# Kernel optimization log

Measured on AMD Instinct MI355X. Metric: run time of the kernel, lower is better.

The kernel has to match this reference:

```python
import jax, jax.numpy as jnp
import numpy as np

N_CLASSES = 64
TRANSDUCTIVE_STEPS = 5


def setup_inputs() -> dict:
    key = jax.random.key(0)
    k1, k2, k3, k4 = jax.random.split(key, 4)
    support = jax.random.normal(k1, (1280, 2048), dtype=jnp.float32)
    query = jax.random.normal(k2, (65536, 2048), dtype=jnp.float32)
    support_labels = jax.random.randint(k3, (1280,), 0, N_CLASSES)
    W_enc = jax.random.normal(k4, (2048, 1024), dtype=jnp.float32) * 0.02
    b_enc = jnp.zeros((1024,), dtype=jnp.float32)
    return {"support": support, "query": query, "support_labels": support_labels,
            "W_enc": W_enc, "b_enc": b_enc}


def _segment_mean(emb, labels, n_seg):
    # masked-mean per class; empty classes stay zero (sum=0 / 1)
    sums = jax.ops.segment_sum(emb, labels, num_segments=n_seg)
    counts = jax.ops.segment_sum(jnp.ones((emb.shape[0],), emb.dtype), labels,
                                 num_segments=n_seg)
    return sums / jnp.maximum(counts, 1.0)[:, None]


def _cdist(x, p):
    # euclidean distance [n, d] x [c, d] -> [n, c]
    d2 = (jnp.sum(x * x, -1)[:, None] + jnp.sum(p * p, -1)[None, :]
          - 2.0 * x @ p.T)
    return jnp.sqrt(jnp.maximum(d2, 1e-12))


def reference(support, query, support_labels, W_enc, b_enc):
    support_emb = support @ W_enc + b_enc   # [ns, d]
    query_emb = query @ W_enc + b_enc       # [nq, d]

    prototypes = _segment_mean(support_emb, support_labels, N_CLASSES)
    all_emb = jnp.concatenate([support_emb, query_emb], axis=0)
    for _ in range(TRANSDUCTIVE_STEPS):
        query_labels = jnp.argmin(_cdist(query_emb, prototypes), axis=-1)
        all_labels = jnp.concatenate([support_labels, query_labels], axis=0)
        prototypes = _segment_mean(all_emb, all_labels, N_CLASSES)

    logits = -_cdist(query_emb, prototypes)  # [nq, n_classes]
    return logits
```

## Files before the change

### kernel.cpp

```cpp
#include <hip/hip_runtime.h>
#include <hip/hip_bf16.h>

#define NS 1280
#define NQ 65536
#define NA (NS + NQ)
#define DIN 2048
#define DEMB 1024
#define NC 64
#define STEPS 5
#define NDBLK (NQ / 128)

typedef __attribute__((ext_vector_type(8))) __bf16 bf16x8;
typedef __attribute__((ext_vector_type(4))) float f32x4;
typedef unsigned short u16;

__device__ __forceinline__ float b2f(u16 u) {
  return __uint_as_float(((unsigned int)u) << 16);
}
__device__ __forceinline__ u16 f2b(float f) {
  __hip_bfloat16 h = __float2bfloat16(f);
  u16 u; __builtin_memcpy(&u, &h, 2); return u;
}
__device__ __forceinline__ void gld_lds16(const void* g, void* l) {
  __builtin_amdgcn_global_load_lds(
      (const __attribute__((address_space(1))) void*)g,
      (__attribute__((address_space(3))) void*)l, 16, 0, 0);
}

__global__ __launch_bounds__(256) void cvt_bf16(const float4* __restrict__ in,
                                                ushort4* __restrict__ out, int n4) {
  for (int i = blockIdx.x * 256 + threadIdx.x; i < n4; i += gridDim.x * 256) {
    float4 v = in[i];
    ushort4 o;
    o.x = f2b(v.x); o.y = f2b(v.y); o.z = f2b(v.z); o.w = f2b(v.w);
    out[i] = o;
  }
}

__global__ __launch_bounds__(256) void transpose_w(const float* __restrict__ W,
                                                   u16* __restrict__ Wt) {
  __shared__ float tile[32][33];
  const int bx = blockIdx.x;
  const int by = blockIdx.y;
  const int tx = threadIdx.x & 31, ty = threadIdx.x >> 5;
#pragma unroll
  for (int j = 0; j < 4; j++)
    tile[ty + 8 * j][tx] = W[(size_t)(by * 32 + ty + 8 * j) * DEMB + bx * 32 + tx];
  __syncthreads();
#pragma unroll
  for (int j = 0; j < 4; j++)
    Wt[(size_t)(bx * 32 + ty + 8 * j) * DIN + by * 32 + tx] = f2b(tile[tx][ty + 8 * j]);
}

__global__ __launch_bounds__(256) void encoder_gemm(const u16* __restrict__ A,
                                                    const u16* __restrict__ Bt,
                                                    const float* __restrict__ bias,
                                                    u16* __restrict__ C) {
  const int b = blockIdx.x;
  const int x = b & 7, tt = b >> 3;
  const int mblk = x + 8 * (tt >> 3);
  const int nblk = tt & 7;
  if (mblk >= NA / 128) return;

  __shared__ u16 As[128 * 32];
  __shared__ u16 Bs[128 * 32];
  const int m0 = mblk * 128, n0 = nblk * 128;
  const int t = threadIdx.x;
  const int w = t >> 6, l = t & 63;
  const int lr = l & 15, lk = (l >> 4) * 8;
  const int wm = (w >> 1) * 64, wn = (w & 1) * 64;

  f32x4 acc[4][4];
  f32x4 z; z.x = 0.f; z.y = 0.f; z.z = 0.f; z.w = 0.f;
#pragma unroll
  for (int i = 0; i < 4; i++)
#pragma unroll
    for (int j = 0; j < 4; j++) acc[i][j] = z;

  const int rA0 = t >> 2, k8 = (t & 3) * 8;
  const u16* gA = A + (size_t)(m0 + rA0) * DIN + k8;
  const u16* gB = Bt + (size_t)(n0 + rA0) * DIN + k8;
  u16* lA = As + t * 8;
  u16* lB = Bs + t * 8;

  for (int kb = 0; kb < DIN; kb += 32) {
    gld_lds16(gA + kb, lA);
    gld_lds16(gA + kb + (size_t)64 * DIN, lA + 64 * 32);
    gld_lds16(gB + kb, lB);
    gld_lds16(gB + kb + (size_t)64 * DIN, lB + 64 * 32);
    __syncthreads();
    bf16x8 af[4], bf[4];
#pragma unroll
    for (int mt = 0; mt < 4; mt++) af[mt] = *(const bf16x8*)&As[(wm + mt * 16 + lr) * 32 + lk];
#pragma unroll
    for (int nt = 0; nt < 4; nt++) bf[nt] = *(const bf16x8*)&Bs[(wn + nt * 16 + lr) * 32 + lk];
#pragma unroll
    for (int mt = 0; mt < 4; mt++)
#pragma unroll
      for (int nt = 0; nt < 4; nt++)
        acc[mt][nt] = __builtin_amdgcn_mfma_f32_16x16x32_bf16(af[mt], bf[nt], acc[mt][nt], 0, 0, 0);
    __syncthreads();
  }
#pragma unroll
  for (int mt = 0; mt < 4; mt++)
#pragma unroll
    for (int nt = 0; nt < 4; nt++)
#pragma unroll
      for (int r = 0; r < 4; r++) {
        int row = m0 + wm + mt * 16 + (l >> 4) * 4 + r;
        int col = n0 + wn + nt * 16 + lr;
        float v = acc[mt][nt][r] + bias[col];
        C[(size_t)row * DEMB + col] = f2b(v);
      }
}

__global__ __launch_bounds__(256) void support_sums(const u16* __restrict__ emb,
                                                    const int* __restrict__ slab,
                                                    float* __restrict__ ssum,
                                                    int* __restrict__ scount) {
  const int c = blockIdx.x, t = threadIdx.x;
  __shared__ int lab[NS];
  for (int i = t; i < NS; i += 256) lab[i] = slab[i];
  __syncthreads();
  float a0 = 0, a1 = 0, a2 = 0, a3 = 0;
  int cnt = 0;
  for (int i = 0; i < NS; i++) {
    if (lab[i] == c) {
      ushort4 e = *(const ushort4*)&emb[(size_t)i * DEMB + t * 4];
      a0 += b2f(e.x); a1 += b2f(e.y); a2 += b2f(e.z); a3 += b2f(e.w);
      cnt++;
    }
  }
  float* dst = ssum + (size_t)c * DEMB + t * 4;
  dst[0] = a0; dst[1] = a1; dst[2] = a2; dst[3] = a3;
  if (t == 0) scount[c] = cnt;
}

__global__ __launch_bounds__(256) void qnorm_kernel(const u16* __restrict__ Q,
                                                    float* __restrict__ qnorm) {
  const int t = threadIdx.x, w = t >> 6, l = t & 63;
  const int row = blockIdx.x * 4 + w;
  const u16* p = Q + (size_t)row * DEMB;
  float s = 0.f;
#pragma unroll
  for (int kk = 0; kk < 4; kk++) {
    ushort4 e = *(const ushort4*)&p[kk * 256 + l * 4];
    float x0 = b2f(e.x), x1 = b2f(e.y), x2 = b2f(e.z), x3 = b2f(e.w);
    s += x0 * x0 + x1 * x1 + x2 * x2 + x3 * x3;
  }
#pragma unroll
  for (int d = 32; d >= 1; d >>= 1) s += __shfl_xor(s, d);
  if (l == 0) qnorm[row] = s;
}

template <bool INIT>
__global__ __launch_bounds__(256) void finalize_protos(const float* __restrict__ ssum,
                                                       const int* __restrict__ scount,
                                                       const float* __restrict__ qpart,
                                                       const int* __restrict__ histpart,
                                                       u16* __restrict__ protos,
                                                       float* __restrict__ pnorm) {
  const int c = blockIdx.x, t = threadIdx.x;
  __shared__ int wredi[4];
  __shared__ float wredf[4];
  __shared__ int cnt_sh;
  float inv;
  if (INIT) {
    inv = 1.0f / fmaxf((float)scount[c], 1.0f);
  } else {
    int p = histpart[(size_t)c * NDBLK + t] + histpart[(size_t)c * NDBLK + 256 + t];
#pragma unroll
    for (int d = 32; d >= 1; d >>= 1) p += __shfl_xor(p, d);
    if ((t & 63) == 0) wredi[t >> 6] = p;
    __syncthreads();
    if (t == 0) cnt_sh = scount[c] + wredi[0] + wredi[1] + wredi[2] + wredi[3];
    __syncthreads();
    inv = 1.0f / fmaxf((float)cnt_sh, 1.0f);
  }
  float part = 0.f;
#pragma unroll
  for (int j = 0; j < 4; j++) {
    const int d = t * 4 + j;
    float v = ssum[(size_t)c * DEMB + d];
    if (!INIT) {
#pragma unroll
      for (int ch = 0; ch < 8; ch++)
        v += qpart[((size_t)ch * NC + c) * DEMB + d];
    }
    v *= inv;
    u16 bits = f2b(v);
    protos[(size_t)c * DEMB + d] = bits;
    float vb = b2f(bits);
    part += vb * vb;
  }
#pragma unroll
  for (int d = 32; d >= 1; d >>= 1) part += __shfl_xor(part, d);
  if ((t & 63) == 0) wredf[t >> 6] = part;
  __syncthreads();
  if (t == 0) pnorm[c] = wredf[0] + wredf[1] + wredf[2] + wredf[3];
}

template <int MODE>
__global__ __launch_bounds__(256) void dist_kernel(const u16* __restrict__ Q,
                                                   const u16* __restrict__ P,
                                                   const float* __restrict__ pnorm,
                                                   const float* __restrict__ qnorm,
                                                   int* __restrict__ labels,
                                                   int* __restrict__ histpart,
                                                   float* __restrict__ out) {
  __shared__ u16 As[128 * 32];
  __shared__ u16 Bs[64 * 32];
  __shared__ int hist[NC];
  const int t = threadIdx.x;
  if (MODE == 0 && t < NC) hist[t] = 0;
  const int m0 = blockIdx.x * 128;
  const int w = t >> 6, l = t & 63;
  const int lr = l & 15, lk = (l >> 4) * 8;
  const int wm = w * 32;

  f32x4 acc[2][4];
  f32x4 z; z.x = 0.f; z.y = 0.f; z.z = 0.f; z.w = 0.f;
#pragma unroll
  for (int i = 0; i < 2; i++)
#pragma unroll
    for (int j = 0; j < 4; j++) acc[i][j] = z;

  const int rA0 = t >> 2, k8 = (t & 3) * 8;
  const u16* gA = Q + (size_t)(m0 + rA0) * DEMB + k8;
  const u16* gB = P + (size_t)rA0 * DEMB + k8;
  u16* lA = As + t * 8;
  u16* lB = Bs + t * 8;

  for (int kb = 0; kb < DEMB; kb += 32) {
    gld_lds16(gA + kb, lA);
    gld_lds16(gA + kb + (size_t)64 * DEMB, lA + 64 * 32);
    gld_lds16(gB + kb, lB);
    __syncthreads();
    bf16x8 af[2], bf[4];
#pragma unroll
    for (int mt = 0; mt < 2; mt++) af[mt] = *(const bf16x8*)&As[(wm + mt * 16 + lr) * 32 + lk];
#pragma unroll
    for (int nt = 0; nt < 4; nt++) bf[nt] = *(const bf16x8*)&Bs[(nt * 16 + lr) * 32 + lk];
#pragma unroll
    for (int mt = 0; mt < 2; mt++)
#pragma unroll
      for (int nt = 0; nt < 4; nt++)
        acc[mt][nt] = __builtin_amdgcn_mfma_f32_16x16x32_bf16(af[mt], bf[nt], acc[mt][nt], 0, 0, 0);
    __syncthreads();
  }

  if (MODE == 0) {
#pragma unroll
    for (int mt = 0; mt < 2; mt++)
#pragma unroll
      for (int r = 0; r < 4; r++) {
        float best = 3.402e38f; int bc = 0;
#pragma unroll
        for (int nt = 0; nt < 4; nt++) {
          int col = nt * 16 + lr;
          float v = pnorm[col] - 2.0f * acc[mt][nt][r];
          if (v < best) { best = v; bc = col; }
        }
#pragma unroll
        for (int s = 1; s < 16; s <<= 1) {
          float ov = __shfl_xor(best, s);
          int oc = __shfl_xor(bc, s);
          if (ov < best || (ov == best && oc < bc)) { best = ov; bc = oc; }
        }
        if (lr == 0) {
          int row = m0 + wm + mt * 16 + (l >> 4) * 4 + r;
          labels[row] = bc;
          atomicAdd(&hist[bc], 1);
        }
      }
    __syncthreads();
    if (t < NC) histpart[(size_t)t * NDBLK + blockIdx.x] = hist[t];
  } else {
#pragma unroll
    for (int mt = 0; mt < 2; mt++)
#pragma unroll
      for (int nt = 0; nt < 4; nt++)
#pragma unroll
        for (int r = 0; r < 4; r++) {
          int row = m0 + wm + mt * 16 + (l >> 4) * 4 + r;
          int col = nt * 16 + lr;
          float d2 = qnorm[row] + pnorm[col] - 2.0f * acc[mt][nt][r];
          out[(size_t)row * NC + col] = -sqrtf(fmaxf(d2, 1e-12f));
        }
  }
}

__global__ __launch_bounds__(256) void class_gather_sum(const u16* __restrict__ Q,
                                                        const int* __restrict__ labels,
                                                        float* __restrict__ qpart) {
  const int c = blockIdx.x >> 3;
  const int chunk = blockIdx.x & 7;
  const int base = chunk * (NQ / 8);
  const int t = threadIdx.x;
  __shared__ int list[NQ / 8];
  __shared__ int nmatch;
  if (t == 0) nmatch = 0;
  __syncthreads();
  for (int i = t; i < NQ / 8; i += 256) {
    if (labels[base + i] == c) {
      int p = atomicAdd(&nmatch, 1);
      list[p] = base + i;
    }
  }
  __syncthreads();
  const int cnt = nmatch;
  float a0 = 0, a1 = 0, a2 = 0, a3 = 0;
  for (int j = 0; j < cnt; j++) {
    int row = list[j];
    ushort4 e = *(const ushort4*)&Q[(size_t)row * DEMB + t * 4];
    a0 += b2f(e.x); a1 += b2f(e.y); a2 += b2f(e.z); a3 += b2f(e.w);
  }
  float* dst = qpart + ((size_t)chunk * NC + c) * DEMB + t * 4;
  dst[0] = a0; dst[1] = a1; dst[2] = a2; dst[3] = a3;
}

extern "C" void kernel_launch(void* const* d_in, const int* in_sizes, int n_in,
                              void* d_out, int out_size, void* d_ws, size_t ws_size,
                              hipStream_t stream) {
  const float* support = (const float*)d_in[0];
  const float* query   = (const float*)d_in[1];
  const int*   slab    = (const int*)d_in[2];
  const float* W       = (const float*)d_in[3];
  const float* bias    = (const float*)d_in[4];
  float* out = (float*)d_out;

  u16* Abf = (u16*)d_ws;
  u16* Wt  = Abf + (size_t)NA * DIN;
  u16* emb = Wt + (size_t)DEMB * DIN;
  float* ssum  = (float*)(emb + (size_t)NA * DEMB);
  float* pnorm = ssum + (size_t)NC * DEMB;
  float* qnorm = pnorm + NC;
  int* scount  = (int*)(qnorm + NQ);
  int* labels  = scount + NC;
  u16* protos  = (u16*)(labels + NQ);
  float* qpart = (float*)Abf;
  int* histpart = (int*)(qpart + (size_t)8 * NC * DEMB);

  const u16* Qemb = emb + (size_t)NS * DEMB;

  cvt_bf16<<<2048, 256, 0, stream>>>((const float4*)support, (ushort4*)Abf,
                                     NS * DIN / 4);
  cvt_bf16<<<8192, 256, 0, stream>>>((const float4*)query,
                                     (ushort4*)(Abf + (size_t)NS * DIN),
                                     NQ * DIN / 4);
  transpose_w<<<dim3(32, 64), 256, 0, stream>>>(W, Wt);

  encoder_gemm<<<8 * 66 * 8, 256, 0, stream>>>(Abf, Wt, bias, emb);

  support_sums<<<NC, 256, 0, stream>>>(emb, slab, ssum, scount);
  qnorm_kernel<<<NQ / 4, 256, 0, stream>>>(Qemb, qnorm);

  finalize_protos<true><<<NC, 256, 0, stream>>>(ssum, scount, qpart, histpart,
                                                protos, pnorm);

  for (int it = 0; it < STEPS; ++it) {
    dist_kernel<0><<<NDBLK, 256, 0, stream>>>(Qemb, protos, pnorm, nullptr,
                                              labels, histpart, nullptr);
    class_gather_sum<<<NC * 8, 256, 0, stream>>>(Qemb, labels, qpart);
    finalize_protos<false><<<NC, 256, 0, stream>>>(ssum, scount, qpart, histpart,
                                                   protos, pnorm);
  }

  dist_kernel<1><<<NDBLK, 256, 0, stream>>>(Qemb, protos, pnorm, qnorm,
                                            nullptr, nullptr, out);
}
```

Before: 1.532 ms.

## Rewrite encoder GEMM with 256x256 tiles, double-buffered swizzled LDS and interleaved prefetch

The encoder GEMM moves from 128x128 tiles with 256 threads and a K-step of 32 to 256x256 tiles with 512 threads and a K-step of 64. Shared memory is double-buffered with XOR-swizzled layout, and the next tile's global-to-LDS loads are interleaved between MFMA phases using explicit waitcnt, barriers and setprio. The aim is more reuse per loaded byte, fewer LDS bank conflicts, and hiding load latency behind compute. In exchange it uses 128KB of LDS and more registers per block, which lowers occupancy, and the hand-placed barrier scheduling is fragile.

```diff
diff --git a/kernel.cpp b/kernel.cpp
--- a/kernel.cpp
+++ b/kernel.cpp
@@ -52,66 +52,142 @@
     Wt[(size_t)(bx * 32 + ty + 8 * j) * DIN + by * 32 + tx] = f2b(tile[tx][ty + 8 * j]);
 }
 
-__global__ __launch_bounds__(256) void encoder_gemm(const u16* __restrict__ A,
-                                                    const u16* __restrict__ Bt,
-                                                    const float* __restrict__ bias,
-                                                    u16* __restrict__ C) {
+__device__ __forceinline__ void mm16(const bf16x8 af[4], const bf16x8 bf[4],
+                                     f32x4 (&acc)[4][4]) {
+#pragma unroll
+  for (int mt = 0; mt < 4; ++mt)
+#pragma unroll
+    for (int nt = 0; nt < 4; ++nt)
+      acc[mt][nt] = __builtin_amdgcn_mfma_f32_16x16x32_bf16(af[mt], bf[nt],
+                                                            acc[mt][nt], 0, 0, 0);
+}
+
+__global__ __launch_bounds__(512, 2) void encoder_gemm(const u16* __restrict__ A,
+                                                       const u16* __restrict__ Bt,
+                                                       const float* __restrict__ bias,
+                                                       u16* __restrict__ C) {
   const int b = blockIdx.x;
   const int x = b & 7, tt = b >> 3;
-  const int mblk = x + 8 * (tt >> 3);
-  const int nblk = tt & 7;
-  if (mblk >= NA / 128) return;
-
-  __shared__ u16 As[128 * 32];
-  __shared__ u16 Bs[128 * 32];
-  const int m0 = mblk * 128, n0 = nblk * 128;
+  const int mblk = x + 8 * (tt >> 2);
+  const int nblk = tt & 3;
+  if (mblk >= NA / 256) return;
+
+  __shared__ u16 lds[65536];
+
+  const int m0 = mblk * 256, n0 = nblk * 256;
   const int t = threadIdx.x;
   const int w = t >> 6, l = t & 63;
-  const int lr = l & 15, lk = (l >> 4) * 8;
-  const int wm = (w >> 1) * 64, wn = (w & 1) * 64;
-
-  f32x4 acc[4][4];
+  const int wm = (w >> 2) * 128;
+  const int wn = (w & 3) * 64;
+  const int lr = l & 15, lk8 = (l >> 4) * 8;
+  const int swz = (lr & 7) << 3;
+
+  const int c1 = t + 512;
+  const int r0 = t >> 3, r1 = c1 >> 3;
+  const int sc0 = (((t & 7) ^ (r0 & 7)) << 3);
+  const int sc1 = (((c1 & 7) ^ (r1 & 7)) << 3);
+
+  const u16* gAt = A + (size_t)m0 * DIN;
+  const u16* gBt = Bt + (size_t)n0 * DIN;
+
+  f32x4 acc[2][4][4];
   f32x4 z; z.x = 0.f; z.y = 0.f; z.z = 0.f; z.w = 0.f;
 #pragma unroll
-  for (int i = 0; i < 4; i++)
-#pragma unroll
-    for (int j = 0; j < 4; j++) acc[i][j] = z;
-
-  const int rA0 = t >> 2, k8 = (t & 3) * 8;
-  const u16* gA = A + (size_t)(m0 + rA0) * DIN + k8;
-  const u16* gB = Bt + (size_t)(n0 + rA0) * DIN + k8;
-  u16* lA = As + t * 8;
-  u16* lB = Bs + t * 8;
-
-  for (int kb = 0; kb < DIN; kb += 32) {
-    gld_lds16(gA + kb, lA);
-    gld_lds16(gA + kb + (size_t)64 * DIN, lA + 64 * 32);
-    gld_lds16(gB + kb, lB);
-    gld_lds16(gB + kb + (size_t)64 * DIN, lB + 64 * 32);
-    __syncthreads();
-    bf16x8 af[4], bf[4];
-#pragma unroll
-    for (int mt = 0; mt < 4; mt++) af[mt] = *(const bf16x8*)&As[(wm + mt * 16 + lr) * 32 + lk];
-#pragma unroll
-    for (int nt = 0; nt < 4; nt++) bf[nt] = *(const bf16x8*)&Bs[(wn + nt * 16 + lr) * 32 + lk];
-#pragma unroll
-    for (int mt = 0; mt < 4; mt++)
-#pragma unroll
-      for (int nt = 0; nt < 4; nt++)
-        acc[mt][nt] = __builtin_amdgcn_mfma_f32_16x16x32_bf16(af[mt], bf[nt], acc[mt][nt], 0, 0, 0);
-    __syncthreads();
-  }
-#pragma unroll
-  for (int mt = 0; mt < 4; mt++)
-#pragma unroll
-    for (int nt = 0; nt < 4; nt++)
-#pragma unroll
-      for (int r = 0; r < 4; r++) {
-        int row = m0 + wm + mt * 16 + (l >> 4) * 4 + r;
-        int col = n0 + wn + nt * 16 + lr;
-        float v = acc[mt][nt][r] + bias[col];
-        C[(size_t)row * DEMB + col] = f2b(v);
-      }
+  for (int g = 0; g < 2; ++g)
+#pragma unroll
+    for (int i = 0; i < 4; ++i)
+#pragma unroll
+      for (int j = 0; j < 4; ++j) acc[g][i][j] = z;
+
+  auto STAGE = [&](const u16* g, u16* S, int h, int kb) {
+    gld_lds16(g + (size_t)(h * 128 + r0) * DIN + kb + sc0, S + h * 8192 + t * 8);
+    gld_lds16(g + (size_t)(h * 128 + r1) * DIN + kb + sc1, S + h * 8192 + c1 * 8);
+  };
+
+  STAGE(gAt, lds, 0, 0);
+  STAGE(gAt, lds, 1, 0);
+  STAGE(gBt, lds + 16384, 0, 0);
+  STAGE(gBt, lds + 16384, 1, 0);
+
+  const int NT = DIN / 64;
+  for (int tk = 0; tk < NT; ++tk) {
+    const int p = tk & 1;
+    u16* LA = lds + p * 32768;
+    u16* LB = LA + 16384;
+    u16* SA = lds + (p ^ 1) * 32768;
+    u16* SB = SA + 16384;
+    const int kbn = (tk + 1) * 64;
+    const bool pre = (tk + 1 < NT);
+
+    bf16x8 af[4], bf0[4], bf1[4];
+
+    if (pre) {
+      STAGE(gAt, SA, 0, kbn);
+      asm volatile("s_waitcnt vmcnt(2)" ::: "memory");
+    } else {
+      asm volatile("s_waitcnt vmcnt(0)" ::: "memory");
+    }
+    __builtin_amdgcn_s_barrier();
+#pragma unroll
+    for (int mt = 0; mt < 4; ++mt)
+      af[mt] = *(const bf16x8*)&LA[(wm + mt * 16 + lr) * 64 + (lk8 ^ swz)];
+#pragma unroll
+    for (int nt = 0; nt < 4; ++nt)
+      bf0[nt] = *(const bf16x8*)&LB[(wn + nt * 16 + lr) * 64 + (lk8 ^ swz)];
+    __builtin_amdgcn_s_setprio(1);
+    mm16(af, bf0, acc[0]);
+    __builtin_amdgcn_s_setprio(0);
+    __builtin_amdgcn_s_barrier();
+
+#pragma unroll
+    for (int mt = 0; mt < 4; ++mt)
+      af[mt] = *(const bf16x8*)&LA[(wm + 64 + mt * 16 + lr) * 64 + (lk8 ^ swz)];
+    if (pre) STAGE(gAt, SA, 1, kbn);
+    __builtin_amdgcn_s_barrier();
+    __builtin_amdgcn_s_setprio(1);
+    mm16(af, bf0, acc[1]);
+    __builtin_amdgcn_s_setprio(0);
+    __builtin_amdgcn_s_barrier();
+
+#pragma unroll
+    for (int mt = 0; mt < 4; ++mt)
+      af[mt] = *(const bf16x8*)&LA[(wm + mt * 16 + lr) * 64 + ((32 + lk8) ^ swz)];
+#pragma unroll
+    for (int nt = 0; nt < 4; ++nt)
+      bf1[nt] = *(const bf16x8*)&LB[(wn + nt * 16 + lr) * 64 + ((32 + lk8) ^ swz)];
+    if (pre) STAGE(gBt, SB, 0, kbn);
+    __builtin_amdgcn_s_barrier();
+    __builtin_amdgcn_s_setprio(1);
+    mm16(af, bf1, acc[0]);
+    __builtin_amdgcn_s_setprio(0);
+    __builtin_amdgcn_s_barrier();
+
+#pragma unroll
+    for (int mt = 0; mt < 4; ++mt)
+      af[mt] = *(const bf16x8*)&LA[(wm + 64 + mt * 16 + lr) * 64 + ((32 + lk8) ^ swz)];
+    if (pre) STAGE(gBt, SB, 1, kbn);
+    __builtin_amdgcn_s_barrier();
+    __builtin_amdgcn_s_setprio(1);
+    mm16(af, bf1, acc[1]);
+    __builtin_amdgcn_s_setprio(0);
+    __builtin_amdgcn_s_barrier();
+  }
+
+  float bv[4];
+#pragma unroll
+  for (int nt = 0; nt < 4; ++nt) bv[nt] = bias[n0 + wn + nt * 16 + lr];
+#pragma unroll
+  for (int mg = 0; mg < 2; ++mg)
+#pragma unroll
+    for (int mt = 0; mt < 4; ++mt)
+#pragma unroll
+      for (int nt = 0; nt < 4; ++nt)
+#pragma unroll
+        for (int r = 0; r < 4; ++r) {
+          int row = m0 + wm + mg * 64 + mt * 16 + (l >> 4) * 4 + r;
+          int col = n0 + wn + nt * 16 + lr;
+          C[(size_t)row * DEMB + col] = f2b(acc[mg][mt][nt][r] + bv[nt]);
+        }
 }
 
 __global__ __launch_bounds__(256) void support_sums(const u16* __restrict__ emb,
@@ -350,7 +426,7 @@
                                      NQ * DIN / 4);
   transpose_w<<<dim3(32, 64), 256, 0, stream>>>(W, Wt);
 
-  encoder_gemm<<<8 * 66 * 8, 256, 0, stream>>>(Abf, Wt, bias, emb);
+  encoder_gemm<<<8 * 33 * 4, 512, 0, stream>>>(Abf, Wt, bias, emb);
 
   support_sums<<<NC, 256, 0, stream>>>(emb, slab, ssum, scount);
   qnorm_kernel<<<NQ / 4, 256, 0, stream>>>(Qemb, qnorm);
```

Result: faster. 1.440 ms (-6.0%).
